# Optimization experiments

Hardware: AMD Instinct MI355X
Metric: run time of the kernel (lower is better)

Reference implementation:

```python
import jax, jax.numpy as jnp
import numpy as np

N_NODES = 100000
N_EDGES = 1600000
HID = 128
EPS = 1e-5

def _bn(x, gamma, beta):
    # BatchNorm1d in training mode: biased batch stats over node dim
    mu = jnp.mean(x, axis=0)
    var = jnp.mean((x - mu) ** 2, axis=0)
    return (x - mu) * jax.lax.rsqrt(var + EPS) * gamma + beta

def _gcn(x, src, dst, norm, n, W, b):
    # PyG GCNConv: h = x @ W, symmetric-normalized aggregation with self-loops, + bias
    h = x @ W
    msg = h[src] * norm[:, None]            # [E+N, H] gather + scale
    out = jax.ops.segment_sum(msg, dst, num_segments=n)
    return out + b

def _gcn_norm(edge_index, n):
    # append self-loops, compute D^{-1/2}[src] * D^{-1/2}[dst]
    loop = jnp.arange(n, dtype=edge_index.dtype)
    src = jnp.concatenate([edge_index[0], loop])
    dst = jnp.concatenate([edge_index[1], loop])
    deg = jax.ops.segment_sum(jnp.ones_like(dst, dtype=jnp.float32), dst, num_segments=n)
    dinv = jax.lax.rsqrt(jnp.maximum(deg, 1.0))  # deg >= 1 due to self loops
    norm = dinv[src] * dinv[dst]
    return src, dst, norm

def setup_inputs() -> dict:
    key = jax.random.key(0)
    ks = jax.random.split(key, 20)
    def lin(k, fan_in, fan_out):
        bound = 1.0 / np.sqrt(fan_in)
        kw, kb = jax.random.split(k)
        W = jax.random.uniform(kw, (fan_in, fan_out), jnp.float32, -bound, bound)
        b = jax.random.uniform(kb, (fan_out,), jnp.float32, -bound, bound)
        return W, b
    x = jax.random.normal(ks[0], (N_NODES, 2), jnp.float32)
    edge_index = jax.random.randint(ks[1], (2, N_EDGES), 0, N_NODES, jnp.int32)
    We, be = lin(ks[2], 2, HID)
    W1, b1 = lin(ks[3], HID, HID)
    W2, b2 = lin(ks[4], HID, HID)
    W3, b3 = lin(ks[5], HID, HID)
    Wf1, bf1 = lin(ks[6], HID, 32)
    Wf2, bf2 = lin(ks[7], 32, 2)
    ones = lambda n: jnp.ones((n,), jnp.float32)
    zeros = lambda n: jnp.zeros((n,), jnp.float32)
    return dict(x=x, edge_index=edge_index, We=We, be=be,
                W1=W1, b1=b1, g1=ones(HID), bt1=zeros(HID),
                W2=W2, b2=b2, g2=ones(HID), bt2=zeros(HID),
                W3=W3, b3=b3, g3=ones(HID), bt3=zeros(HID),
                Wf1=Wf1, bf1=bf1, gf=ones(32), btf=zeros(32),
                Wf2=Wf2, bf2=bf2)

def reference(x, edge_index, We, be, W1, b1, g1, bt1, W2, b2, g2, bt2,
              W3, b3, g3, bt3, Wf1, bf1, gf, btf, Wf2, bf2):
    n = x.shape[0]
    src, dst, norm = _gcn_norm(edge_index, n)
    h = jax.nn.relu(x @ We + be)
    # block 1 with residual
    h1 = jax.nn.relu(_bn(_gcn(h, src, dst, norm, n, W1, b1), g1, bt1)) + h
    # block 2
    h2 = jax.nn.relu(_bn(_gcn(h1, src, dst, norm, n, W2, b2), g2, bt2)) + h1
    # block 3
    h3 = jax.nn.relu(_bn(_gcn(h2, src, dst, norm, n, W3, b3), g3, bt3)) + h2
    f = jax.nn.relu(_bn(h3 @ Wf1 + bf1, gf, btf))
    # dropout is identity in eval mode
    return jnp.tanh(f @ Wf2 + bf2)
```

## Files before the change

kernel.cpp:

```cpp
#include <hip/hip_runtime.h>
#include <hip/hip_fp16.h>
#include <math.h>

#define HID 128
#define EPS 1e-5f
#define BK 64
#define MAXNBK 2048
#define NSTRIPE 16
#define PADK 136

typedef _Float16 half8 __attribute__((ext_vector_type(8)));
typedef float f32x4 __attribute__((ext_vector_type(4)));


__global__ __launch_bounds__(256) void k_bhist(const int* __restrict__ dst, int* __restrict__ bcount,
                                               int e, int nbk) {
    __shared__ int hist[MAXNBK];
    for (int i = threadIdx.x; i < nbk; i += 256) hist[i] = 0;
    __syncthreads();
    int base = blockIdx.x * 4096;
    int end = min(base + 4096, e);
    for (int i = base + threadIdx.x; i < end; i += 256) atomicAdd(&hist[dst[i] >> 6], 1);
    __syncthreads();
    for (int i = threadIdx.x; i < nbk; i += 256) {
        int c = hist[i];
        if (c) atomicAdd(&bcount[i * 16], c);
    }
}

__global__ __launch_bounds__(1024) void k_bscan(const int* __restrict__ bcount, int* __restrict__ boffs,
                                                int* __restrict__ bcur, int nbk, int e) {
    __shared__ int lds[1024];
    int tid = threadIdx.x;
    int i0 = 2 * tid, i1 = 2 * tid + 1;
    int a = (i0 < nbk) ? bcount[i0 * 16] : 0;
    int b = (i1 < nbk) ? bcount[i1 * 16] : 0;
    lds[tid] = a + b;
    __syncthreads();
    for (int off = 1; off < 1024; off <<= 1) {
        int v = (tid >= off) ? lds[tid - off] : 0;
        __syncthreads();
        lds[tid] += v;
        __syncthreads();
    }
    int excl = lds[tid] - (a + b);
    if (i0 < nbk) { boffs[i0] = excl;     bcur[i0 * 16] = excl; }
    if (i1 < nbk) { boffs[i1] = excl + a; bcur[i1 * 16] = excl + a; }
    if (tid == 1023) boffs[nbk] = e;
}

__global__ __launch_bounds__(1024) void k_bscatter(const int* __restrict__ src, const int* __restrict__ dst,
                                                   int* __restrict__ bcur, int* __restrict__ btmp,
                                                   int e, int nbk) {
    __shared__ int hist[MAXNBK];
    int tid = threadIdx.x;
    for (int i = tid; i < nbk; i += 1024) hist[i] = 0;
    __syncthreads();
    int per = (e + gridDim.x - 1) / gridDim.x;
    int base = blockIdx.x * per;
    int end = min(base + per, e);
    for (int i = base + tid; i < end; i += 1024) atomicAdd(&hist[dst[i] >> 6], 1);
    __syncthreads();
    for (int i = tid; i < nbk; i += 1024) {
        int c = hist[i];
        hist[i] = c ? atomicAdd(&bcur[i * 16], c) : 0;
    }
    __syncthreads();
    for (int i = base + tid; i < end; i += 1024) {
        int d = dst[i];
        int pos = atomicAdd(&hist[d >> 6], 1);
        btmp[pos] = (src[i] << 6) | (d & 63);
    }
}

__global__ __launch_bounds__(256) void k_bsort(const int* __restrict__ btmp, const int* __restrict__ boffs,
                                               int* __restrict__ csr, int* __restrict__ offs,
                                               float* __restrict__ dinv, int n, int etot) {
    __shared__ int cnt[BK];
    __shared__ int cur[BK];
    int b = blockIdx.x, tid = threadIdx.x;
    if (tid < BK) cnt[tid] = 0;
    __syncthreads();
    int e0 = boffs[b], e1 = boffs[b + 1];
    for (int i = e0 + tid; i < e1; i += 256) atomicAdd(&cnt[btmp[i] & 63], 1);
    __syncthreads();
    if (tid == 0) {
        int run = 0;
        for (int d = 0; d < BK; ++d) { cur[d] = run; run += cnt[d]; }
    }
    __syncthreads();
    if (tid < BK) {
        int node = b * BK + tid;
        if (node < n) {
            offs[node] = e0 + cur[tid];
            dinv[node] = rsqrtf((float)(cnt[tid] + 1));
        }
    }
    if (b == 0 && tid == 0) offs[n] = etot;
    __syncthreads();
    for (int i = e0 + tid; i < e1; i += 256) {
        int p = btmp[i];
        int pos = e0 + atomicAdd(&cur[p & 63], 1);
        csr[pos] = p >> 6;
    }
}


__global__ void k_prepw(const float* __restrict__ W, _Float16* __restrict__ Wt) {
    int idx = blockIdx.x * 256 + threadIdx.x;
    int k = idx >> 7, nn = idx & 127;
    Wt[nn * 128 + k] = (_Float16)W[k * 128 + nn];
}

__global__ void k_prepwf(const float* __restrict__ W, _Float16* __restrict__ Wt) {
    int idx = blockIdx.x * 256 + threadIdx.x;
    int k = idx >> 5, nn = idx & 31;
    Wt[nn * 128 + k] = (_Float16)W[k * 32 + nn];
}


__global__ __launch_bounds__(256) void k_mm1(const float* __restrict__ x, const float* __restrict__ We,
                                             const float* __restrict__ be, const _Float16* __restrict__ Wt,
                                             const float* __restrict__ dinv, __half2* __restrict__ th,
                                             __half2* __restrict__ h, int n) {
    __shared__ __attribute__((aligned(16))) _Float16 Ah[64][PADK];
    __shared__ __attribute__((aligned(16))) _Float16 Bh[128][PADK];
    __shared__ float W0s[128], W1s[128], bes[128];
    int tid = threadIdx.x;
    int nb = blockIdx.x * 64;
    if (tid < 128) { W0s[tid] = We[tid]; W1s[tid] = We[128 + tid]; bes[tid] = be[tid]; }
    __syncthreads();
    uint2* h2p = (uint2*)h;
    const float2* x2 = (const float2*)x;
#pragma unroll
    for (int r = 0; r < 8; ++r) {
        int idx = r * 256 + tid;
        int ni = idx >> 5, k4 = idx & 31;
        int node = nb + ni;
        float4 v = make_float4(0.f, 0.f, 0.f, 0.f);
        union { __half2 h2[2]; uint2 u; } pk;
        if (node < n) {
            float2 xx = x2[node];
            float4 w0 = *((const float4*)&W0s[k4 * 4]);
            float4 w1 = *((const float4*)&W1s[k4 * 4]);
            float4 bb = *((const float4*)&bes[k4 * 4]);
            v.x = fmaxf(xx.x * w0.x + xx.y * w1.x + bb.x, 0.f);
            v.y = fmaxf(xx.x * w0.y + xx.y * w1.y + bb.y, 0.f);
            v.z = fmaxf(xx.x * w0.z + xx.y * w1.z + bb.z, 0.f);
            v.w = fmaxf(xx.x * w0.w + xx.y * w1.w + bb.w, 0.f);
            pk.h2[0] = __floats2half2_rn(v.x, v.y);
            pk.h2[1] = __floats2half2_rn(v.z, v.w);
            h2p[(size_t)node * 32 + k4] = pk.u;
        } else {
            pk.h2[0] = __floats2half2_rn(0.f, 0.f);
            pk.h2[1] = __floats2half2_rn(0.f, 0.f);
        }
        *(uint2*)&Ah[ni][k4 * 4] = pk.u;
    }
    const uint4* wt4 = (const uint4*)Wt;
#pragma unroll
    for (int r = 0; r < 8; ++r) {
        int idx = r * 256 + tid;
        int row = idx >> 4, ch = idx & 15;
        *(uint4*)&Bh[row][ch * 8] = wt4[row * 16 + ch];
    }
    __syncthreads();
    int lane = tid & 63, w = tid >> 6;
    int mrow = lane & 15, quad = lane >> 4;
    f32x4 acc[8];
#pragma unroll
    for (int t = 0; t < 8; ++t) acc[t] = (f32x4){0.f, 0.f, 0.f, 0.f};
#pragma unroll
    for (int kc = 0; kc < 4; ++kc) {
        half8 av = *(half8*)&Ah[w * 16 + mrow][kc * 32 + quad * 8];
#pragma unroll
        for (int t = 0; t < 8; ++t) {
            half8 bv = *(half8*)&Bh[t * 16 + mrow][kc * 32 + quad * 8];
            acc[t] = __builtin_amdgcn_mfma_f32_16x16x32_f16(av, bv, acc[t], 0, 0, 0);
        }
    }
    float dv[4];
#pragma unroll
    for (int r = 0; r < 4; ++r) {
        int node = nb + w * 16 + quad * 4 + r;
        dv[r] = (node < n) ? dinv[node] : 0.f;
    }
    __syncthreads();
#pragma unroll
    for (int t = 0; t < 8; ++t)
#pragma unroll
        for (int r = 0; r < 4; ++r)
            Ah[w * 16 + quad * 4 + r][t * 16 + mrow] = (_Float16)(acc[t][r] * dv[r]);
    __syncthreads();
#pragma unroll
    for (int it = 0; it < 4; ++it) {
        int idx = it * 256 + tid;
        int row = idx >> 4, ch = idx & 15;
        int node = nb + row;
        if (node < n)
            ((uint4*)th)[(size_t)node * 16 + ch] = *(uint4*)&Ah[row][ch * 8];
    }
}


__global__ __launch_bounds__(256) void k_mmf(const __half2* __restrict__ agg, __half2* __restrict__ h,
                                             const float* __restrict__ S, const float* __restrict__ SS,
                                             const float* __restrict__ g, const float* __restrict__ bt,
                                             const _Float16* __restrict__ Wt, const float* __restrict__ dinv,
                                             __half2* __restrict__ th, int n) {
    __shared__ __attribute__((aligned(16))) _Float16 Ah[64][PADK];
    __shared__ __attribute__((aligned(16))) _Float16 Bh[128][PADK];
    __shared__ float As[128], Cs[128];
    int tid = threadIdx.x;
    int nb = blockIdx.x * 64;
    if (tid < 128) {
        float s = 0.f, q = 0.f;
#pragma unroll
        for (int k = 0; k < NSTRIPE; ++k) { s += S[k * 128 + tid]; q += SS[k * 128 + tid]; }
        float mu = s / (float)n;
        float var = q / (float)n - mu * mu;
        float inv = rsqrtf(var + EPS);
        As[tid] = g[tid] * inv;
        Cs[tid] = bt[tid] - mu * g[tid] * inv;
    }
    __syncthreads();
    const uint2* a2p = (const uint2*)agg;
    uint2* h2p = (uint2*)h;
#pragma unroll
    for (int r = 0; r < 8; ++r) {
        int idx = r * 256 + tid;
        int ni = idx >> 5, k4 = idx & 31;
        int node = nb + ni;
        union { __half2 h2[2]; uint2 u; } pk;
        if (node < n) {
            uint2 au = a2p[(size_t)node * 32 + k4];
            uint2 hu = h2p[(size_t)node * 32 + k4];
            float2 a01 = __half22float2(*(__half2*)&au.x);
            float2 a23 = __half22float2(*(__half2*)&au.y);
            float2 h01 = __half22float2(*(__half2*)&hu.x);
            float2 h23 = __half22float2(*(__half2*)&hu.y);
            float4 aa = *((const float4*)&As[k4 * 4]);
            float4 cc = *((const float4*)&Cs[k4 * 4]);
            float v0 = fmaxf(a01.x * aa.x + cc.x, 0.f) + h01.x;
            float v1 = fmaxf(a01.y * aa.y + cc.y, 0.f) + h01.y;
            float v2 = fmaxf(a23.x * aa.z + cc.z, 0.f) + h23.x;
            float v3 = fmaxf(a23.y * aa.w + cc.w, 0.f) + h23.y;
            pk.h2[0] = __floats2half2_rn(v0, v1);
            pk.h2[1] = __floats2half2_rn(v2, v3);
            h2p[(size_t)node * 32 + k4] = pk.u;
        } else {
            pk.h2[0] = __floats2half2_rn(0.f, 0.f);
            pk.h2[1] = __floats2half2_rn(0.f, 0.f);
        }
        *(uint2*)&Ah[ni][k4 * 4] = pk.u;
    }
    const uint4* wt4 = (const uint4*)Wt;
#pragma unroll
    for (int r = 0; r < 8; ++r) {
        int idx = r * 256 + tid;
        int row = idx >> 4, ch = idx & 15;
        *(uint4*)&Bh[row][ch * 8] = wt4[row * 16 + ch];
    }
    __syncthreads();
    int lane = tid & 63, w = tid >> 6;
    int mrow = lane & 15, quad = lane >> 4;
    f32x4 acc[8];
#pragma unroll
    for (int t = 0; t < 8; ++t) acc[t] = (f32x4){0.f, 0.f, 0.f, 0.f};
#pragma unroll
    for (int kc = 0; kc < 4; ++kc) {
        half8 av = *(half8*)&Ah[w * 16 + mrow][kc * 32 + quad * 8];
#pragma unroll
        for (int t = 0; t < 8; ++t) {
            half8 bv = *(half8*)&Bh[t * 16 + mrow][kc * 32 + quad * 8];
            acc[t] = __builtin_amdgcn_mfma_f32_16x16x32_f16(av, bv, acc[t], 0, 0, 0);
        }
    }
    float dv[4];
#pragma unroll
    for (int r = 0; r < 4; ++r) {
        int node = nb + w * 16 + quad * 4 + r;
        dv[r] = (node < n) ? dinv[node] : 0.f;
    }
    __syncthreads();
#pragma unroll
    for (int t = 0; t < 8; ++t)
#pragma unroll
        for (int r = 0; r < 4; ++r)
            Ah[w * 16 + quad * 4 + r][t * 16 + mrow] = (_Float16)(acc[t][r] * dv[r]);
    __syncthreads();
#pragma unroll
    for (int it = 0; it < 4; ++it) {
        int idx = it * 256 + tid;
        int row = idx >> 4, ch = idx & 15;
        int node = nb + row;
        if (node < n)
            ((uint4*)th)[(size_t)node * 16 + ch] = *(uint4*)&Ah[row][ch * 8];
    }
}


__global__ __launch_bounds__(256) void k_mmh(const __half2* __restrict__ agg, const __half2* __restrict__ h,
                                             const float* __restrict__ Sin, const float* __restrict__ SSin,
                                             const float* __restrict__ g, const float* __restrict__ bt,
                                             const _Float16* __restrict__ Wt, const float* __restrict__ bias,
                                             float* __restrict__ tf,
                                             float* __restrict__ S, float* __restrict__ SS, int n) {
    __shared__ __attribute__((aligned(16))) _Float16 Ah[64][PADK];
    __shared__ __attribute__((aligned(16))) _Float16 Bh[32][PADK];
    __shared__ float Ds[64][36];
    __shared__ float As[128], Cs[128];
    __shared__ float sredS[4][8][4], sredQ[4][8][4];
    int tid = threadIdx.x;
    int nb = blockIdx.x * 64;
    if (tid < 128) {
        float s = 0.f, q = 0.f;
#pragma unroll
        for (int k = 0; k < NSTRIPE; ++k) { s += Sin[k * 128 + tid]; q += SSin[k * 128 + tid]; }
        float mu = s / (float)n;
        float var = q / (float)n - mu * mu;
        float inv = rsqrtf(var + EPS);
        As[tid] = g[tid] * inv;
        Cs[tid] = bt[tid] - mu * g[tid] * inv;
    }
    __syncthreads();
    const uint2* a2p = (const uint2*)agg;
    const uint2* h2p = (const uint2*)h;
#pragma unroll
    for (int r = 0; r < 8; ++r) {
        int idx = r * 256 + tid;
        int ni = idx >> 5, k4 = idx & 31;
        int node = nb + ni;
        union { __half2 h2[2]; uint2 u; } pk;
        if (node < n) {
            uint2 au = a2p[(size_t)node * 32 + k4];
            uint2 hu = h2p[(size_t)node * 32 + k4];
            float2 a01 = __half22float2(*(__half2*)&au.x);
            float2 a23 = __half22float2(*(__half2*)&au.y);
            float2 h01 = __half22float2(*(__half2*)&hu.x);
            float2 h23 = __half22float2(*(__half2*)&hu.y);
            float4 aa = *((const float4*)&As[k4 * 4]);
            float4 cc = *((const float4*)&Cs[k4 * 4]);
            float v0 = fmaxf(a01.x * aa.x + cc.x, 0.f) + h01.x;
            float v1 = fmaxf(a01.y * aa.y + cc.y, 0.f) + h01.y;
            float v2 = fmaxf(a23.x * aa.z + cc.z, 0.f) + h23.x;
            float v3 = fmaxf(a23.y * aa.w + cc.w, 0.f) + h23.y;
            pk.h2[0] = __floats2half2_rn(v0, v1);
            pk.h2[1] = __floats2half2_rn(v2, v3);
        } else {
            pk.h2[0] = __floats2half2_rn(0.f, 0.f);
            pk.h2[1] = __floats2half2_rn(0.f, 0.f);
        }
        *(uint2*)&Ah[ni][k4 * 4] = pk.u;
    }
    const uint4* wt4 = (const uint4*)Wt;
#pragma unroll
    for (int r = 0; r < 2; ++r) {
        int idx = r * 256 + tid;
        int row = idx >> 4, ch = idx & 15;
        *(uint4*)&Bh[row][ch * 8] = wt4[row * 16 + ch];
    }
    __syncthreads();
    int lane = tid & 63, w = tid >> 6;
    int mrow = lane & 15, quad = lane >> 4;
    f32x4 acc[2];
    acc[0] = (f32x4){0.f, 0.f, 0.f, 0.f};
    acc[1] = (f32x4){0.f, 0.f, 0.f, 0.f};
#pragma unroll
    for (int kc = 0; kc < 4; ++kc) {
        half8 av = *(half8*)&Ah[w * 16 + mrow][kc * 32 + quad * 8];
#pragma unroll
        for (int t = 0; t < 2; ++t) {
            half8 bv = *(half8*)&Bh[t * 16 + mrow][kc * 32 + quad * 8];
            acc[t] = __builtin_amdgcn_mfma_f32_16x16x32_f16(av, bv, acc[t], 0, 0, 0);
        }
    }
#pragma unroll
    for (int t = 0; t < 2; ++t)
#pragma unroll
        for (int r = 0; r < 4; ++r)
            Ds[w * 16 + quad * 4 + r][t * 16 + mrow] = acc[t][r];
    __syncthreads();
    float ps0 = 0.f, ps1 = 0.f, ps2 = 0.f, ps3 = 0.f;
    float pq0 = 0.f, pq1 = 0.f, pq2 = 0.f, pq3 = 0.f;
    int c4 = tid & 7;
    float4 bb = ((const float4*)bias)[c4];
#pragma unroll
    for (int it = 0; it < 2; ++it) {
        int idx = it * 256 + tid;
        int row = idx >> 3;
        int node = nb + row;
        if (node < n) {
            float v0 = Ds[row][c4 * 4 + 0] + bb.x;
            float v1 = Ds[row][c4 * 4 + 1] + bb.y;
            float v2 = Ds[row][c4 * 4 + 2] + bb.z;
            float v3 = Ds[row][c4 * 4 + 3] + bb.w;
            *((float4*)&tf[(size_t)node * 32 + c4 * 4]) = make_float4(v0, v1, v2, v3);
            ps0 += v0; ps1 += v1; ps2 += v2; ps3 += v3;
            pq0 += v0 * v0; pq1 += v1 * v1; pq2 += v2 * v2; pq3 += v3 * v3;
        }
    }
#pragma unroll
    for (int off = 8; off < 64; off <<= 1) {
        ps0 += __shfl_down(ps0, off); ps1 += __shfl_down(ps1, off);
        ps2 += __shfl_down(ps2, off); ps3 += __shfl_down(ps3, off);
        pq0 += __shfl_down(pq0, off); pq1 += __shfl_down(pq1, off);
        pq2 += __shfl_down(pq2, off); pq3 += __shfl_down(pq3, off);
    }
    if (lane < 8) {
        sredS[w][lane][0] = ps0; sredS[w][lane][1] = ps1; sredS[w][lane][2] = ps2; sredS[w][lane][3] = ps3;
        sredQ[w][lane][0] = pq0; sredQ[w][lane][1] = pq1; sredQ[w][lane][2] = pq2; sredQ[w][lane][3] = pq3;
    }
    __syncthreads();
    if (tid < 32) {
        int cc4 = tid >> 2, j = tid & 3;
        float s = sredS[0][cc4][j] + sredS[1][cc4][j] + sredS[2][cc4][j] + sredS[3][cc4][j];
        float q = sredQ[0][cc4][j] + sredQ[1][cc4][j] + sredQ[2][cc4][j] + sredQ[3][cc4][j];
        int stripe = (blockIdx.x & (NSTRIPE - 1)) * 128;
        atomicAdd(&S[stripe + tid], s);
        atomicAdd(&SS[stripe + tid], q);
    }
}


__global__ __launch_bounds__(256) void k_agg(const __half2* __restrict__ t, const int* __restrict__ offs,
                                             const int* __restrict__ csr, const float* __restrict__ dinv,
                                             const float* __restrict__ bias, __half2* __restrict__ out,
                                             float* __restrict__ S, float* __restrict__ SS, int n) {
    __shared__ float ls[4][128];
    __shared__ float lss[4][128];
    int tid = threadIdx.x;
    int lane = tid & 63, w = tid >> 6;
    int sub = lane >> 5, fl = lane & 31;
    const uint2* t4 = (const uint2*)t;
    float4 bb = ((const float4*)bias)[fl];
    float s0 = 0.f, s1 = 0.f, s2 = 0.f, s3 = 0.f;
    float q0 = 0.f, q1 = 0.f, q2 = 0.f, q3 = 0.f;
    float selfm = (sub == 0) ? 1.f : 0.f;
    int ngrp = (n + 3) >> 2;
    for (int grp = blockIdx.x; grp < ngrp; grp += gridDim.x) {
        int node = grp * 4 + w;
        if (node < n) {
            uint2 rv = t4[(size_t)node * 32 + fl];
            float2 f0 = __half22float2(*(__half2*)&rv.x);
            float2 f1 = __half22float2(*(__half2*)&rv.y);
            float a0 = f0.x * selfm, a1 = f0.y * selfm, a2 = f1.x * selfm, a3 = f1.y * selfm;
            int e0 = offs[node], e1 = offs[node + 1];
            for (int e = e0; e < e1; e += 8) {
                int i0 = e + sub, i1 = e + 2 + sub, i2 = e + 4 + sub, i3 = e + 6 + sub;
                int c0 = csr[min(i0, e1 - 1)];
                int c1 = csr[min(i1, e1 - 1)];
                int c2 = csr[min(i2, e1 - 1)];
                int c3 = csr[min(i3, e1 - 1)];
                uint2 r0 = t4[(size_t)c0 * 32 + fl];
                uint2 r1 = t4[(size_t)c1 * 32 + fl];
                uint2 r2 = t4[(size_t)c2 * 32 + fl];
                uint2 r3 = t4[(size_t)c3 * 32 + fl];
                float m0 = (i0 < e1) ? 1.f : 0.f;
                float m1 = (i1 < e1) ? 1.f : 0.f;
                float m2 = (i2 < e1) ? 1.f : 0.f;
                float m3 = (i3 < e1) ? 1.f : 0.f;
                float2 g0 = __half22float2(*(__half2*)&r0.x), g1 = __half22float2(*(__half2*)&r0.y);
                a0 += m0 * g0.x; a1 += m0 * g0.y; a2 += m0 * g1.x; a3 += m0 * g1.y;
                g0 = __half22float2(*(__half2*)&r1.x); g1 = __half22float2(*(__half2*)&r1.y);
                a0 += m1 * g0.x; a1 += m1 * g0.y; a2 += m1 * g1.x; a3 += m1 * g1.y;
                g0 = __half22float2(*(__half2*)&r2.x); g1 = __half22float2(*(__half2*)&r2.y);
                a0 += m2 * g0.x; a1 += m2 * g0.y; a2 += m2 * g1.x; a3 += m2 * g1.y;
                g0 = __half22float2(*(__half2*)&r3.x); g1 = __half22float2(*(__half2*)&r3.y);
                a0 += m3 * g0.x; a1 += m3 * g0.y; a2 += m3 * g1.x; a3 += m3 * g1.y;
            }
            a0 += __shfl_down(a0, 32);
            a1 += __shfl_down(a1, 32);
            a2 += __shfl_down(a2, 32);
            a3 += __shfl_down(a3, 32);
            if (sub == 0) {
                float di = dinv[node];
                float v0 = a0 * di + bb.x, v1 = a1 * di + bb.y;
                float v2 = a2 * di + bb.z, v3 = a3 * di + bb.w;
                union { __half2 h2[2]; uint2 u; } pk;
                pk.h2[0] = __floats2half2_rn(v0, v1);
                pk.h2[1] = __floats2half2_rn(v2, v3);
                ((uint2*)out)[(size_t)node * 32 + fl] = pk.u;
                s0 += v0; s1 += v1; s2 += v2; s3 += v3;
                q0 += v0 * v0; q1 += v1 * v1; q2 += v2 * v2; q3 += v3 * v3;
            }
        }
    }
    if (sub == 0) {
        ((float4*)&ls[w][0])[fl] = make_float4(s0, s1, s2, s3);
        ((float4*)&lss[w][0])[fl] = make_float4(q0, q1, q2, q3);
    }
    __syncthreads();
    if (tid < 128) {
        float s = ls[0][tid] + ls[1][tid] + ls[2][tid] + ls[3][tid];
        float q = lss[0][tid] + lss[1][tid] + lss[2][tid] + lss[3][tid];
        int stripe = (blockIdx.x & (NSTRIPE - 1)) * 128;
        atomicAdd(&S[stripe + tid], s);
        atomicAdd(&SS[stripe + tid], q);
    }
}


__global__ __launch_bounds__(256) void k_final(const float* __restrict__ tf,
                                               const float* __restrict__ S, const float* __restrict__ SS,
                                               const float* __restrict__ gf, const float* __restrict__ btf,
                                               const float* __restrict__ Wf2, const float* __restrict__ bf2,
                                               float* __restrict__ out, int n) {
    __shared__ float Af[32], Cf[32];
    int tid = threadIdx.x;
    if (tid < 32) {
        float s = 0.f, q = 0.f;
#pragma unroll
        for (int k = 0; k < NSTRIPE; ++k) { s += S[k * 128 + tid]; q += SS[k * 128 + tid]; }
        float mu = s / (float)n;
        float var = q / (float)n - mu * mu;
        float inv = rsqrtf(var + EPS);
        Af[tid] = gf[tid] * inv;
        Cf[tid] = btf[tid] - mu * gf[tid] * inv;
    }
    __syncthreads();
    int node = blockIdx.x * 256 + tid;
    if (node >= n) return;
    float o0 = bf2[0], o1 = bf2[1];
    const float4* t4 = (const float4*)(tf + (size_t)node * 32);
#pragma unroll
    for (int q = 0; q < 8; ++q) {
        float4 v = t4[q];
        float vv[4] = {v.x, v.y, v.z, v.w};
#pragma unroll
        for (int r = 0; r < 4; ++r) {
            int j = q * 4 + r;
            float f = fmaxf(vv[r] * Af[j] + Cf[j], 0.f);
            o0 += f * Wf2[2 * j];
            o1 += f * Wf2[2 * j + 1];
        }
    }
    out[2 * node] = tanhf(o0);
    out[2 * node + 1] = tanhf(o1);
}


extern "C" void kernel_launch(void* const* d_in, const int* in_sizes, int n_in,
                              void* d_out, int out_size, void* d_ws, size_t ws_size,
                              hipStream_t stream) {
    const float* x   = (const float*)d_in[0];
    const int*   ei  = (const int*)d_in[1];
    const float* We  = (const float*)d_in[2];
    const float* be  = (const float*)d_in[3];
    const float* W1  = (const float*)d_in[4];
    const float* b1  = (const float*)d_in[5];
    const float* g1  = (const float*)d_in[6];
    const float* bt1 = (const float*)d_in[7];
    const float* W2  = (const float*)d_in[8];
    const float* b2  = (const float*)d_in[9];
    const float* g2  = (const float*)d_in[10];
    const float* bt2 = (const float*)d_in[11];
    const float* W3  = (const float*)d_in[12];
    const float* b3  = (const float*)d_in[13];
    const float* g3  = (const float*)d_in[14];
    const float* bt3 = (const float*)d_in[15];
    const float* Wf1 = (const float*)d_in[16];
    const float* bf1 = (const float*)d_in[17];
    const float* gf  = (const float*)d_in[18];
    const float* btf = (const float*)d_in[19];
    const float* Wf2 = (const float*)d_in[20];
    const float* bf2 = (const float*)d_in[21];
    float* out = (float*)d_out;

    const int n = in_sizes[0] / 2;
    const int e = in_sizes[1] / 2;
    const int* srcp = ei;
    const int* dstp = ei + e;
    const int nbk = (n + BK - 1) / BK;

    char* p = (char*)d_ws;
    auto alloc = [&](size_t bytes) { void* r = (void*)p; p += (bytes + 255) & ~(size_t)255; return r; };
    int*       bcount = (int*)alloc((size_t)nbk * 16 * 4);
    int*       boffs  = (int*)alloc((size_t)(nbk + 1) * 4);
    int*       bcur   = (int*)alloc((size_t)nbk * 16 * 4);
    int*       btmp   = (int*)alloc((size_t)e * 4);
    int*       csr    = (int*)alloc((size_t)e * 4);
    int*       offs   = (int*)alloc((size_t)(n + 1) * 4);
    float*     dinv   = (float*)alloc((size_t)n * 4);
    __half2*   h      = (__half2*)alloc((size_t)n * HID * 2);
    __half2*   th     = (__half2*)alloc((size_t)n * HID * 2);
    __half2*   agg    = (__half2*)alloc((size_t)n * HID * 2);
    float*     tf     = (float*)alloc((size_t)n * 32 * 4);
    float*     bnAll  = (float*)alloc(8 * NSTRIPE * 128 * 4);
    _Float16*  wt1    = (_Float16*)alloc(128 * 128 * 2);
    _Float16*  wt2    = (_Float16*)alloc(128 * 128 * 2);
    _Float16*  wt3    = (_Float16*)alloc(128 * 128 * 2);
    _Float16*  wtf    = (_Float16*)alloc(32 * 128 * 2);

    float* S0 = bnAll;             float* SS0 = bnAll + 4 * NSTRIPE * 128;
    float* S1 = S0 + NSTRIPE*128;  float* SS1 = SS0 + NSTRIPE*128;
    float* S2 = S1 + NSTRIPE*128;  float* SS2 = SS1 + NSTRIPE*128;
    float* SH = S2 + NSTRIPE*128;  float* SSH = SS2 + NSTRIPE*128;

    hipMemsetAsync(bcount, 0, (size_t)nbk * 16 * 4, stream);
    hipMemsetAsync(bnAll, 0, 8 * NSTRIPE * 128 * 4, stream);
    k_bhist<<<(e + 4095) / 4096, 256, 0, stream>>>(dstp, bcount, e, nbk);
    k_bscan<<<1, 1024, 0, stream>>>(bcount, boffs, bcur, nbk, e);
    k_bscatter<<<256, 1024, 0, stream>>>(srcp, dstp, bcur, btmp, e, nbk);
    k_bsort<<<nbk, 256, 0, stream>>>(btmp, boffs, csr, offs, dinv, n, e);
    k_prepw<<<64, 256, 0, stream>>>(W1, wt1);
    k_prepw<<<64, 256, 0, stream>>>(W2, wt2);
    k_prepw<<<64, 256, 0, stream>>>(W3, wt3);
    k_prepwf<<<16, 256, 0, stream>>>(Wf1, wtf);

    k_mm1<<<(n + 63) / 64, 256, 0, stream>>>(x, We, be, wt1, dinv, th, h, n);
    k_agg<<<4096, 256, 0, stream>>>(th, offs, csr, dinv, b1, agg, S0, SS0, n);

    k_mmf<<<(n + 63) / 64, 256, 0, stream>>>(agg, h, S0, SS0, g1, bt1, wt2, dinv, th, n);
    k_agg<<<4096, 256, 0, stream>>>(th, offs, csr, dinv, b2, agg, S1, SS1, n);

    k_mmf<<<(n + 63) / 64, 256, 0, stream>>>(agg, h, S1, SS1, g2, bt2, wt3, dinv, th, n);
    k_agg<<<4096, 256, 0, stream>>>(th, offs, csr, dinv, b3, agg, S2, SS2, n);

    k_mmh<<<(n + 63) / 64, 256, 0, stream>>>(agg, h, S2, SS2, g3, bt3, wtf, bf1, tf, SH, SSH, n);

    k_final<<<(n + 255) / 256, 256, 0, stream>>>(tf, SH, SSH, gf, btf, Wf2, bf2, out, n);
}
```

Baseline: 474.4 us.

## Split aggregation across feature-column groups with 16 edges per wave

Rewrites the CSR aggregation kernel so each block handles one of 8 column groups of 16 features. Each wave processes one node with 16 edge lanes times 4 feature lanes, in place of 2 edge lanes times 32 feature lanes. The aim is more memory-level parallelism per node through more concurrent edge gathers. In exchange, each gather fetches only a 32-byte segment of a row, and the loop now assumes a fixed grid of 512*8 blocks, hardcoding the launch configuration.

```diff
diff --git a/kernel.cpp b/kernel.cpp
--- a/kernel.cpp
+++ b/kernel.cpp
@@ -427,76 +427,68 @@
                                              const int* __restrict__ csr, const float* __restrict__ dinv,
                                              const float* __restrict__ bias, __half2* __restrict__ out,
                                              float* __restrict__ S, float* __restrict__ SS, int n) {
-    __shared__ float ls[4][128];
-    __shared__ float lss[4][128];
+    __shared__ float ls[4][16];
+    __shared__ float lss[4][16];
     int tid = threadIdx.x;
     int lane = tid & 63, w = tid >> 6;
-    int sub = lane >> 5, fl = lane & 31;
+    int g = blockIdx.x & 7;
+    int gb = blockIdx.x >> 3;
+    int es = lane >> 2, fl = lane & 3;
+    int cbase = g * 4 + fl;
     const uint2* t4 = (const uint2*)t;
-    float4 bb = ((const float4*)bias)[fl];
+    float4 bb = ((const float4*)bias)[cbase];
     float s0 = 0.f, s1 = 0.f, s2 = 0.f, s3 = 0.f;
     float q0 = 0.f, q1 = 0.f, q2 = 0.f, q3 = 0.f;
-    float selfm = (sub == 0) ? 1.f : 0.f;
+    float selfm = (es == 0) ? 1.f : 0.f;
     int ngrp = (n + 3) >> 2;
-    for (int grp = blockIdx.x; grp < ngrp; grp += gridDim.x) {
+    for (int grp = gb; grp < ngrp; grp += 512) {
         int node = grp * 4 + w;
         if (node < n) {
-            uint2 rv = t4[(size_t)node * 32 + fl];
+            uint2 rv = t4[(size_t)node * 32 + cbase];
             float2 f0 = __half22float2(*(__half2*)&rv.x);
             float2 f1 = __half22float2(*(__half2*)&rv.y);
             float a0 = f0.x * selfm, a1 = f0.y * selfm, a2 = f1.x * selfm, a3 = f1.y * selfm;
             int e0 = offs[node], e1 = offs[node + 1];
-            for (int e = e0; e < e1; e += 8) {
-                int i0 = e + sub, i1 = e + 2 + sub, i2 = e + 4 + sub, i3 = e + 6 + sub;
-                int c0 = csr[min(i0, e1 - 1)];
-                int c1 = csr[min(i1, e1 - 1)];
-                int c2 = csr[min(i2, e1 - 1)];
-                int c3 = csr[min(i3, e1 - 1)];
-                uint2 r0 = t4[(size_t)c0 * 32 + fl];
-                uint2 r1 = t4[(size_t)c1 * 32 + fl];
-                uint2 r2 = t4[(size_t)c2 * 32 + fl];
-                uint2 r3 = t4[(size_t)c3 * 32 + fl];
-                float m0 = (i0 < e1) ? 1.f : 0.f;
-                float m1 = (i1 < e1) ? 1.f : 0.f;
-                float m2 = (i2 < e1) ? 1.f : 0.f;
-                float m3 = (i3 < e1) ? 1.f : 0.f;
-                float2 g0 = __half22float2(*(__half2*)&r0.x), g1 = __half22float2(*(__half2*)&r0.y);
-                a0 += m0 * g0.x; a1 += m0 * g0.y; a2 += m0 * g1.x; a3 += m0 * g1.y;
-                g0 = __half22float2(*(__half2*)&r1.x); g1 = __half22float2(*(__half2*)&r1.y);
-                a0 += m1 * g0.x; a1 += m1 * g0.y; a2 += m1 * g1.x; a3 += m1 * g1.y;
-                g0 = __half22float2(*(__half2*)&r2.x); g1 = __half22float2(*(__half2*)&r2.y);
-                a0 += m2 * g0.x; a1 += m2 * g0.y; a2 += m2 * g1.x; a3 += m2 * g1.y;
-                g0 = __half22float2(*(__half2*)&r3.x); g1 = __half22float2(*(__half2*)&r3.y);
-                a0 += m3 * g0.x; a1 += m3 * g0.y; a2 += m3 * g1.x; a3 += m3 * g1.y;
+            for (int e = e0; e < e1; e += 16) {
+                int i = e + es;
+                int c = csr[min(i, e1 - 1)];
+                uint2 r = t4[(size_t)c * 32 + cbase];
+                float m = (i < e1) ? 1.f : 0.f;
+                float2 g0 = __half22float2(*(__half2*)&r.x);
+                float2 g1 = __half22float2(*(__half2*)&r.y);
+                a0 += m * g0.x; a1 += m * g0.y; a2 += m * g1.x; a3 += m * g1.y;
             }
-            a0 += __shfl_down(a0, 32);
-            a1 += __shfl_down(a1, 32);
-            a2 += __shfl_down(a2, 32);
-            a3 += __shfl_down(a3, 32);
-            if (sub == 0) {
+#pragma unroll
+            for (int off = 4; off < 64; off <<= 1) {
+                a0 += __shfl_down(a0, off);
+                a1 += __shfl_down(a1, off);
+                a2 += __shfl_down(a2, off);
+                a3 += __shfl_down(a3, off);
+            }
+            if (es == 0) {
                 float di = dinv[node];
                 float v0 = a0 * di + bb.x, v1 = a1 * di + bb.y;
                 float v2 = a2 * di + bb.z, v3 = a3 * di + bb.w;
                 union { __half2 h2[2]; uint2 u; } pk;
                 pk.h2[0] = __floats2half2_rn(v0, v1);
                 pk.h2[1] = __floats2half2_rn(v2, v3);
-                ((uint2*)out)[(size_t)node * 32 + fl] = pk.u;
+                ((uint2*)out)[(size_t)node * 32 + cbase] = pk.u;
                 s0 += v0; s1 += v1; s2 += v2; s3 += v3;
                 q0 += v0 * v0; q1 += v1 * v1; q2 += v2 * v2; q3 += v3 * v3;
             }
         }
     }
-    if (sub == 0) {
-        ((float4*)&ls[w][0])[fl] = make_float4(s0, s1, s2, s3);
-        ((float4*)&lss[w][0])[fl] = make_float4(q0, q1, q2, q3);
-    }
-    __syncthreads();
-    if (tid < 128) {
+    if (es == 0) {
+        *(float4*)&ls[w][fl * 4] = make_float4(s0, s1, s2, s3);
+        *(float4*)&lss[w][fl * 4] = make_float4(q0, q1, q2, q3);
+    }
+    __syncthreads();
+    if (tid < 16) {
         float s = ls[0][tid] + ls[1][tid] + ls[2][tid] + ls[3][tid];
         float q = lss[0][tid] + lss[1][tid] + lss[2][tid] + lss[3][tid];
-        int stripe = (blockIdx.x & (NSTRIPE - 1)) * 128;
-        atomicAdd(&S[stripe + tid], s);
-        atomicAdd(&SS[stripe + tid], q);
+        int stripe = (gb & (NSTRIPE - 1)) * 128;
+        atomicAdd(&S[stripe + g * 16 + tid], s);
+        atomicAdd(&SS[stripe + g * 16 + tid], q);
     }
 }
 
```

Result: slower. 948.0 us (+99.8%).
